# Optimization experiments

Measured on AMD Instinct MI355X. Metric: run time of the kernel, lower is better.

Reference implementation:

```python
import jax, jax.numpy as jnp
import numpy as np

B, C, T, L = 32, 21, 512, 336
FREQ = T // 2 + 1  # 257
EPS = 1e-5


def setup_inputs() -> dict:
    key = jax.random.key(0)
    k1, k2, k3 = jax.random.split(key, 3)
    z = jax.random.normal(k1, (B, C, T), dtype=jnp.float32)
    affine_w = jnp.ones((C,), dtype=jnp.float32)
    affine_b = jnp.zeros((C,), dtype=jnp.float32)
    head_w = jax.random.normal(k2, (L, T * FREQ), dtype=jnp.float32) * 0.002
    head_b = jax.random.normal(k3, (L,), dtype=jnp.float32) * 0.01
    return {"z": z, "affine_w": affine_w, "affine_b": affine_b,
            "head_w": head_w, "head_b": head_b}


def _bases(T, FREQ):
    # t = arange(0,1,1/T); rows p: cos(2*pi*p*t), -sin(2*pi*p*t); DC row scaled by 0.5
    t = jnp.arange(T, dtype=jnp.float32) / T
    p = jnp.arange(FREQ, dtype=jnp.float32)
    ang = 2.0 * jnp.pi * p[:, None] * t[None, :]          # (FREQ, T)
    cosb = jnp.cos(ang).at[0].multiply(0.5)
    sinb = (-jnp.sin(ang)).at[0].multiply(0.5)
    return cosb, sinb


def reference(z, affine_w, affine_b, head_w, head_b):
    # RevIN 'norm' over time axis (unbiased=False variance)
    mean = jnp.mean(z, axis=-1, keepdims=True)              # (B,C,1)
    std = jnp.sqrt(jnp.var(z, axis=-1, keepdims=True) + EPS)
    w = affine_w[None, :, None]
    b = affine_b[None, :, None]
    zn = (z - mean) / std * w + b                           # (B,C,T)

    X = jnp.fft.rfft(zn, axis=-1) / T * 2.0                 # (B,C,FREQ) complex
    cosb, sinb = _bases(T, FREQ)
    # outer-product basis expansion -> (B,C,FREQ,T)
    basis = (jnp.einsum('bcp,pt->bcpt', jnp.real(X), cosb)
             + jnp.einsum('bcp,pt->bcpt', jnp.imag(X), sinb)).astype(jnp.float32)
    flat = basis.reshape(B, C, FREQ * T)                    # (B,C,head_nf)

    out = jnp.einsum('bcn,ln->bcl', flat, head_w) + head_b  # (B,C,L)

    # RevIN 'denorm'
    out = (out - b) / (w + EPS * EPS) * std + mean
    return out
```

## Files before the change

kernel.cpp:

```cpp
#include <hip/hip_runtime.h>
#include <math.h>

#define BB 32
#define CC 21
#define TT 512
#define LL 336
#define FREQ 257
#define NBC (BB*CC)
#define WROW (FREQ*TT)

#define ANG (6.2831853071795864769e0f / 512.0f)

__device__ __forceinline__ float wave_sum(float v) {
#pragma unroll
    for (int off = 32; off; off >>= 1) v += __shfl_xor(v, off);
    return v;
}

__global__ __launch_bounds__(320) void kA_zdft(const float* __restrict__ z,
                                               const float* __restrict__ aw,
                                               const float* __restrict__ ab,
                                               float* __restrict__ ZC,
                                               float* __restrict__ ZS,
                                               float* __restrict__ stats) {
    __shared__ float  zrow[512];
    __shared__ float  zeo[512];
    __shared__ float2 tab[512];
    __shared__ float  red[10];
    const int bc  = blockIdx.x;
    const int tid = threadIdx.x;
    const float* zr = z + (size_t)bc * TT;

    float v0 = zr[tid];
    float v1 = (tid < 192) ? zr[tid + 320] : 0.0f;
    zrow[tid] = v0;
    if (tid < 192) zrow[tid + 320] = v1;

    float s  = v0 + v1;
    float sq = v0 * v0 + v1 * v1;
    s  = wave_sum(s);
    sq = wave_sum(sq);
    const int lane = tid & 63, wv = tid >> 6;
    if (lane == 0) { red[wv] = s; red[5 + wv] = sq; }

    {
        float fk = (float)tid * (1.0f / 256.0f);
        tab[tid] = make_float2(cospif(fk), sinpif(fk));
        if (tid < 192) {
            float fk2 = (float)(tid + 320) * (1.0f / 256.0f);
            tab[tid + 320] = make_float2(cospif(fk2), sinpif(fk2));
        }
    }
    __syncthreads();

    if (tid < 256) {
        float a = zrow[tid], b = zrow[tid + 256];
        zeo[tid]       = a + b;
        zeo[tid + 256] = a - b;
    }
    if (tid == 0) {
        float sum   = red[0]+red[1]+red[2]+red[3]+red[4];
        float sumsq = red[5]+red[6]+red[7]+red[8]+red[9];
        float mu  = sum * (1.0f / 512.0f);
        float var = sumsq * (1.0f / 512.0f) - mu * mu;
        float sg  = sqrtf(var + 1e-5f);
        int c = bc % CC;
        float w = aw[c], b = ab[c];
        *(float4*)(stats + 4 * bc) = make_float4(mu, sg, w / sg, b - w * mu / sg);
    }
    __syncthreads();

    if (tid < FREQ) {
        const int p = tid;
        const float* u = zeo + ((p & 1) ? 256 : 0);
        float ac = 0.f, as = 0.f;
        int k = 0;
#pragma unroll 8
        for (int t = 0; t < 256; ++t) {
            float uv = u[t];
            float2 cs = tab[k];
            ac = fmaf(uv, cs.x, ac);
            as = fmaf(uv, cs.y, as);
            k = (k + p) & 511;
        }
        ZC[bc * FREQ + p] = ac;
        ZS[bc * FREQ + p] = as;
    }
}

__global__ __launch_bounds__(256) void kB_wproj(const float* __restrict__ hw,
                                                float* __restrict__ CA,
                                                float* __restrict__ SA) {
    const int l    = blockIdx.y;
    const int w    = threadIdx.x >> 6;
    const int lane = threadIdx.x & 63;
    const int p    = blockIdx.x * 4 + w;
    if (p >= FREQ) return;

    const float4* src = (const float4*)(hw + (size_t)l * WROW + (size_t)p * TT);
    float4 w1 = src[lane];
    float4 w2 = src[lane + 64];

    const float sgn = (p & 1) ? -1.0f : 1.0f;
    float u0 = fmaf(sgn, w2.x, w1.x);
    float u1 = fmaf(sgn, w2.y, w1.y);
    float u2 = fmaf(sgn, w2.z, w1.z);
    float u3 = fmaf(sgn, w2.w, w1.w);

    const int   k0 = (p * (lane * 4)) & 511;
    const float a0 = (float)k0 * ANG;
    float c0 = __cosf(a0), s0 = __sinf(a0);
    const float ad = (float)p * ANG;
    float cd = __cosf(ad), sd = __sinf(ad);

    float c1 = c0 * cd - s0 * sd, s1 = s0 * cd + c0 * sd;
    float c2 = c1 * cd - s1 * sd, s2 = s1 * cd + c1 * sd;
    float c3 = c2 * cd - s2 * sd, s3 = s2 * cd + c2 * sd;

    float accA = u0 * c0 + u1 * c1 + u2 * c2 + u3 * c3;
    float accB = u0 * s0 + u1 * s1 + u2 * s2 + u3 * s3;
    accA = wave_sum(accA);
    accB = wave_sum(accB);

    if (lane == 0) {
        if (p == 0) { accA *= 0.5f; accB *= 0.5f; }
        CA[p * LL + l] = accA;
        SA[p * LL + l] = accB;
    }
}

__global__ __launch_bounds__(384) void kC_gemm(const float* __restrict__ ZC,
                                               const float* __restrict__ ZS,
                                               const float* __restrict__ CA,
                                               const float* __restrict__ SA,
                                               const float* __restrict__ stats,
                                               const float* __restrict__ aw,
                                               const float* __restrict__ ab,
                                               const float* __restrict__ hb,
                                               float* __restrict__ out) {
    const int l = threadIdx.x;
    if (l >= LL) return;
    const int bc0 = blockIdx.x * 4;
    const float* zc0 = ZC + (size_t)bc0 * FREQ;
    const float* zs0 = ZS + (size_t)bc0 * FREQ;

    float d0 = 0.f, d1 = 0.f, d2 = 0.f, d3 = 0.f;
#pragma unroll 4
    for (int p = 0; p < FREQ; ++p) {
        float ca = CA[p * LL + l];
        float sa = SA[p * LL + l];
        d0 = fmaf(zc0[p],            ca, fmaf(zs0[p],            sa, d0));
        d1 = fmaf(zc0[FREQ + p],     ca, fmaf(zs0[FREQ + p],     sa, d1));
        d2 = fmaf(zc0[2 * FREQ + p], ca, fmaf(zs0[2 * FREQ + p], sa, d2));
        d3 = fmaf(zc0[3 * FREQ + p], ca, fmaf(zs0[3 * FREQ + p], sa, d3));
    }
    const float ca0 = CA[l];
    const float hbl = hb[l];
    float d[4] = {d0, d1, d2, d3};
#pragma unroll
    for (int j = 0; j < 4; ++j) {
        int bc = bc0 + j;
        int c  = bc % CC;
        float mu = stats[4 * bc + 0];
        float sg = stats[4 * bc + 1];
        float ga = stats[4 * bc + 2];
        float de = stats[4 * bc + 3];
        float pre = fmaf(ga * d[j], 2.0f / 512.0f, fmaf(2.0f * de, ca0, hbl));
        out[(size_t)bc * LL + l] = (pre - ab[c]) / (aw[c] + 1e-10f) * sg + mu;
    }
}

extern "C" void kernel_launch(void* const* d_in, const int* in_sizes, int n_in,
                              void* d_out, int out_size, void* d_ws, size_t ws_size,
                              hipStream_t stream) {
    const float* z  = (const float*)d_in[0];
    const float* aw = (const float*)d_in[1];
    const float* ab = (const float*)d_in[2];
    const float* hw = (const float*)d_in[3];
    const float* hb = (const float*)d_in[4];
    float* out = (float*)d_out;

    float* ws    = (float*)d_ws;
    float* ZC    = ws;
    float* ZS    = ZC + NBC * FREQ;
    float* CA    = ZS + NBC * FREQ;
    float* SA    = CA + FREQ * LL;
    float* stats = SA + FREQ * LL;

    kB_wproj<<<dim3(65, 336), 256, 0, stream>>>(hw, CA, SA);
    kA_zdft <<<NBC, 320, 0, stream>>>(z, aw, ab, ZC, ZS, stats);
    kC_gemm <<<NBC / 4, 384, 0, stream>>>(ZC, ZS, CA, SA, stats, aw, ab, hb, out);
}
```

Measured before the change: 301.2 us.

## Fuse weight projection and z DFT into one launch, rebalance GEMM grid

```diff
diff --git a/kernel.cpp b/kernel.cpp
--- a/kernel.cpp
+++ b/kernel.cpp
@@ -11,24 +11,73 @@
 
 #define ANG (6.2831853071795864769e0f / 512.0f)
 
+#define PCHUNK 52
+#define KB_BLOCKS (PCHUNK * LL)
+
 __device__ __forceinline__ float wave_sum(float v) {
 #pragma unroll
     for (int off = 32; off; off >>= 1) v += __shfl_xor(v, off);
     return v;
 }
 
-__global__ __launch_bounds__(320) void kA_zdft(const float* __restrict__ z,
-                                               const float* __restrict__ aw,
-                                               const float* __restrict__ ab,
-                                               float* __restrict__ ZC,
-                                               float* __restrict__ ZS,
-                                               float* __restrict__ stats) {
+__global__ __launch_bounds__(320) void k1_fused(const float* __restrict__ z,
+                                                const float* __restrict__ hw,
+                                                const float* __restrict__ aw,
+                                                const float* __restrict__ ab,
+                                                float* __restrict__ ZC,
+                                                float* __restrict__ ZS,
+                                                float* __restrict__ CA,
+                                                float* __restrict__ SA,
+                                                float* __restrict__ stats) {
+    const int tid  = threadIdx.x;
+    const int lane = tid & 63;
+    const int w    = tid >> 6;
+
+    if (blockIdx.x >= NBC) {
+        const int bxx = blockIdx.x - NBC;
+        const int l   = bxx / PCHUNK;
+        const int pc  = bxx - l * PCHUNK;
+        const int p   = pc * 5 + w;
+        if (p >= FREQ) return;
+
+        const float4* src = (const float4*)(hw + (size_t)l * WROW + (size_t)p * TT);
+        float4 w1 = src[lane];
+        float4 w2 = src[lane + 64];
+
+        const float sgn = (p & 1) ? -1.0f : 1.0f;
+        float u0 = fmaf(sgn, w2.x, w1.x);
+        float u1 = fmaf(sgn, w2.y, w1.y);
+        float u2 = fmaf(sgn, w2.z, w1.z);
+        float u3 = fmaf(sgn, w2.w, w1.w);
+
+        const int   k0 = (p * (lane * 4)) & 511;
+        const float a0 = (float)k0 * ANG;
+        float c0 = __cosf(a0), s0 = __sinf(a0);
+        const float ad = (float)p * ANG;
+        float cd = __cosf(ad), sd = __sinf(ad);
+
+        float c1 = c0 * cd - s0 * sd, s1 = s0 * cd + c0 * sd;
+        float c2 = c1 * cd - s1 * sd, s2 = s1 * cd + c1 * sd;
+        float c3 = c2 * cd - s2 * sd, s3 = s2 * cd + c2 * sd;
+
+        float accA = u0 * c0 + u1 * c1 + u2 * c2 + u3 * c3;
+        float accB = u0 * s0 + u1 * s1 + u2 * s2 + u3 * s3;
+        accA = wave_sum(accA);
+        accB = wave_sum(accB);
+
+        if (lane == 0) {
+            if (p == 0) { accA *= 0.5f; accB *= 0.5f; }
+            CA[p * LL + l] = accA;
+            SA[p * LL + l] = accB;
+        }
+        return;
+    }
+
     __shared__ float  zrow[512];
     __shared__ float  zeo[512];
     __shared__ float2 tab[512];
     __shared__ float  red[10];
-    const int bc  = blockIdx.x;
-    const int tid = threadIdx.x;
+    const int bc = blockIdx.x;
     const float* zr = z + (size_t)bc * TT;
 
     float v0 = zr[tid];
@@ -40,8 +89,7 @@
     float sq = v0 * v0 + v1 * v1;
     s  = wave_sum(s);
     sq = wave_sum(sq);
-    const int lane = tid & 63, wv = tid >> 6;
-    if (lane == 0) { red[wv] = s; red[5 + wv] = sq; }
+    if (lane == 0) { red[w] = s; red[5 + w] = sq; }
 
     {
         float fk = (float)tid * (1.0f / 256.0f);
@@ -65,67 +113,34 @@
         float var = sumsq * (1.0f / 512.0f) - mu * mu;
         float sg  = sqrtf(var + 1e-5f);
         int c = bc % CC;
-        float w = aw[c], b = ab[c];
-        *(float4*)(stats + 4 * bc) = make_float4(mu, sg, w / sg, b - w * mu / sg);
+        float ww = aw[c], bb = ab[c];
+        *(float4*)(stats + 4 * bc) = make_float4(mu, sg, ww / sg, bb - ww * mu / sg);
     }
     __syncthreads();
 
     if (tid < FREQ) {
         const int p = tid;
         const float* u = zeo + ((p & 1) ? 256 : 0);
-        float ac = 0.f, as = 0.f;
-        int k = 0;
+        const float ad = (float)p * ANG;
+        const float cd = __cosf(ad), sd = __sinf(ad);
+        float ac = 0.f, as_ = 0.f;
+#pragma unroll
+        for (int ch = 0; ch < 4; ++ch) {
+            const int base = (p * (ch * 64)) & 511;
+            float2 cs = tab[base];
+            float c = cs.x, sn = cs.y;
 #pragma unroll 8
-        for (int t = 0; t < 256; ++t) {
-            float uv = u[t];
-            float2 cs = tab[k];
-            ac = fmaf(uv, cs.x, ac);
-            as = fmaf(uv, cs.y, as);
-            k = (k + p) & 511;
+            for (int j = 0; j < 64; ++j) {
+                float uv = u[ch * 64 + j];
+                ac  = fmaf(uv, c,  ac);
+                as_ = fmaf(uv, sn, as_);
+                float nc = fmaf(c, cd, -(sn * sd));
+                sn = fmaf(sn, cd, c * sd);
+                c  = nc;
+            }
         }
         ZC[bc * FREQ + p] = ac;
-        ZS[bc * FREQ + p] = as;
-    }
-}
-
-__global__ __launch_bounds__(256) void kB_wproj(const float* __restrict__ hw,
-                                                float* __restrict__ CA,
-                                                float* __restrict__ SA) {
-    const int l    = blockIdx.y;
-    const int w    = threadIdx.x >> 6;
-    const int lane = threadIdx.x & 63;
-    const int p    = blockIdx.x * 4 + w;
-    if (p >= FREQ) return;
-
-    const float4* src = (const float4*)(hw + (size_t)l * WROW + (size_t)p * TT);
-    float4 w1 = src[lane];
-    float4 w2 = src[lane + 64];
-
-    const float sgn = (p & 1) ? -1.0f : 1.0f;
-    float u0 = fmaf(sgn, w2.x, w1.x);
-    float u1 = fmaf(sgn, w2.y, w1.y);
-    float u2 = fmaf(sgn, w2.z, w1.z);
-    float u3 = fmaf(sgn, w2.w, w1.w);
-
-    const int   k0 = (p * (lane * 4)) & 511;
-    const float a0 = (float)k0 * ANG;
-    float c0 = __cosf(a0), s0 = __sinf(a0);
-    const float ad = (float)p * ANG;
-    float cd = __cosf(ad), sd = __sinf(ad);
-
-    float c1 = c0 * cd - s0 * sd, s1 = s0 * cd + c0 * sd;
-    float c2 = c1 * cd - s1 * sd, s2 = s1 * cd + c1 * sd;
-    float c3 = c2 * cd - s2 * sd, s3 = s2 * cd + c2 * sd;
-
-    float accA = u0 * c0 + u1 * c1 + u2 * c2 + u3 * c3;
-    float accB = u0 * s0 + u1 * s1 + u2 * s2 + u3 * s3;
-    accA = wave_sum(accA);
-    accB = wave_sum(accB);
-
-    if (lane == 0) {
-        if (p == 0) { accA *= 0.5f; accB *= 0.5f; }
-        CA[p * LL + l] = accA;
-        SA[p * LL + l] = accB;
+        ZS[bc * FREQ + p] = as_;
     }
 }
 
@@ -140,25 +155,27 @@
                                                float* __restrict__ out) {
     const int l = threadIdx.x;
     if (l >= LL) return;
-    const int bc0 = blockIdx.x * 4;
-    const float* zc0 = ZC + (size_t)bc0 * FREQ;
-    const float* zs0 = ZS + (size_t)bc0 * FREQ;
-
-    float d0 = 0.f, d1 = 0.f, d2 = 0.f, d3 = 0.f;
-#pragma unroll 4
+    const int bc0 = blockIdx.x * 2;
+    const float* zcA = ZC + (size_t)bc0 * FREQ;
+    const float* zsA = ZS + (size_t)bc0 * FREQ;
+    const float* zcB = zcA + FREQ;
+    const float* zsB = zsA + FREQ;
+
+    float d0 = 0.f, e0 = 0.f, d1 = 0.f, e1 = 0.f;
+#pragma unroll 8
     for (int p = 0; p < FREQ; ++p) {
         float ca = CA[p * LL + l];
         float sa = SA[p * LL + l];
-        d0 = fmaf(zc0[p],            ca, fmaf(zs0[p],            sa, d0));
-        d1 = fmaf(zc0[FREQ + p],     ca, fmaf(zs0[FREQ + p],     sa, d1));
-        d2 = fmaf(zc0[2 * FREQ + p], ca, fmaf(zs0[2 * FREQ + p], sa, d2));
-        d3 = fmaf(zc0[3 * FREQ + p], ca, fmaf(zs0[3 * FREQ + p], sa, d3));
+        d0 = fmaf(zcA[p], ca, d0);
+        e0 = fmaf(zsA[p], sa, e0);
+        d1 = fmaf(zcB[p], ca, d1);
+        e1 = fmaf(zsB[p], sa, e1);
     }
     const float ca0 = CA[l];
     const float hbl = hb[l];
-    float d[4] = {d0, d1, d2, d3};
+    float d[2] = {d0 + e0, d1 + e1};
 #pragma unroll
-    for (int j = 0; j < 4; ++j) {
+    for (int j = 0; j < 2; ++j) {
         int bc = bc0 + j;
         int c  = bc % CC;
         float mu = stats[4 * bc + 0];
@@ -187,7 +204,6 @@
     float* SA    = CA + FREQ * LL;
     float* stats = SA + FREQ * LL;
 
-    kB_wproj<<<dim3(65, 336), 256, 0, stream>>>(hw, CA, SA);
-    kA_zdft <<<NBC, 320, 0, stream>>>(z, aw, ab, ZC, ZS, stats);
-    kC_gemm <<<NBC / 4, 384, 0, stream>>>(ZC, ZS, CA, SA, stats, aw, ab, hb, out);
-}
+    k1_fused<<<NBC + KB_BLOCKS, 320, 0, stream>>>(z, hw, aw, ab, ZC, ZS, CA, SA, stats);
+    kC_gemm <<<LL, 384, 0, stream>>>(ZC, ZS, CA, SA, stats, aw, ab, hb, out);
+}
```

Result: faster. 274.6 us (-8.8%).
